# Kernel tuning notes

Measured on AMD Instinct MI355X. Metric: run time of the kernel, lower is better.

The kernel has to match this reference:

```python
import jax, jax.numpy as jnp
import numpy as np

B, E, H, N_TAYLOR = 8192, 256, 4096, 4
BN_EPS = 1e-5


def setup_inputs() -> dict:
    key = jax.random.key(0)
    ks = jax.random.split(key, 6)
    s = 0.02
    return {
        "z1": jax.random.normal(ks[0], (B, E), jnp.float32),
        "z2": jax.random.normal(ks[1], (B, E), jnp.float32),
        "p1": jax.random.normal(ks[2], (B, E), jnp.float32),
        "p2": jax.random.normal(ks[3], (B, E), jnp.float32),
        "W1": jax.random.normal(ks[4], (E, H), jnp.float32) * s,
        "gamma": jnp.ones((H,), jnp.float32),
        "beta": jnp.zeros((H,), jnp.float32),
        "W2": jax.random.normal(ks[5], (H, E), jnp.float32) * s,
        "b2": jnp.zeros((E,), jnp.float32),
        "lamda_inv": jnp.asarray(100.0, jnp.float32),
    }


def _predictor(z, W1, gamma, beta, W2, b2):
    h = z @ W1                                   # [B, H]
    mu = jnp.mean(h, axis=0)
    var = jnp.mean(jnp.square(h - mu), axis=0)   # biased var (torch BN training)
    h = (h - mu) * jax.lax.rsqrt(var + BN_EPS) * gamma + beta
    h = jax.nn.relu(h)
    return h @ W2 + b2                           # [B, E]


def _l2norm(x):
    n = jnp.linalg.norm(x, axis=1, keepdims=True)
    return x / jnp.maximum(n, 1e-12)


def _mec(view1, view2, lamda_inv):
    v1, v2 = _l2norm(view1), _l2norm(view2)
    c = (v1 @ v2.T) / lamda_inv                  # [B, B]
    power = c
    sum_p = jnp.zeros_like(c)
    for k in range(1, N_TAYLOR + 1):
        if k > 1:
            power = power @ c
        sign = 1.0 if (k + 1) % 2 == 0 else -1.0
        sum_p = sum_p + sign * power / k
    return jnp.trace(sum_p)


def reference(z1, z2, p1, p2, W1, gamma, beta, W2, b2, lamda_inv):
    q1 = _predictor(z1, W1, gamma, beta, W2, b2)
    q2 = _predictor(z2, W1, gamma, beta, W2, b2)
    loss = (_mec(p1, q2, lamda_inv) + _mec(p2, q1, lamda_inv)) * 0.5 / B
    return -loss * lamda_inv
```

## Files before the change

kernel.cpp:

```cpp
#include <hip/hip_runtime.h>

#define B_ROWS 8192
#define E_DIM  256
#define H_DIM  4096

typedef __attribute__((ext_vector_type(8))) short short8;
typedef __attribute__((ext_vector_type(4))) float f32x4;

typedef __attribute__((address_space(1))) const void* gas1_t;
typedef __attribute__((address_space(3))) void*       las3_t;

__device__ __forceinline__ float b2f(unsigned short s) {
    return __uint_as_float(((unsigned)s) << 16);
}
__device__ __forceinline__ unsigned short f2b(float f) {
    unsigned u = __float_as_uint(f);
    u += 0x7fffu + ((u >> 16) & 1u);
    return (unsigned short)(u >> 16);
}

__device__ __forceinline__ int swz(int row, int slot) {
    return slot ^ ((row >> 1) & 3);
}

__global__ void k_transpose_cast(const float* __restrict__ in,
                                 unsigned short* __restrict__ out,
                                 int R, int C) {
    __shared__ float tile[32][33];
    const int c0 = blockIdx.x * 32, r0 = blockIdx.y * 32;
    const int tx = threadIdx.x & 31, ty = threadIdx.x >> 5;
#pragma unroll
    for (int j = 0; j < 4; ++j)
        tile[ty * 4 + j][tx] = in[(size_t)(r0 + ty * 4 + j) * C + c0 + tx];
    __syncthreads();
#pragma unroll
    for (int j = 0; j < 4; ++j)
        out[(size_t)(c0 + ty * 4 + j) * R + r0 + tx] = f2b(tile[tx][ty * 4 + j]);
}

__global__ void k_cast_bf16(const float* __restrict__ in,
                            unsigned short* __restrict__ out, int n4) {
    int i = blockIdx.x * blockDim.x + threadIdx.x;
    if (i < n4) {
        float4 v = ((const float4*)in)[i];
        ushort4 o;
        o.x = f2b(v.x); o.y = f2b(v.y); o.z = f2b(v.z); o.w = f2b(v.w);
        ((ushort4*)out)[i] = o;
    }
}

__global__ __launch_bounds__(256) void k_gemm1(
    const unsigned short* __restrict__ A, const unsigned short* __restrict__ Bt,
    unsigned short* __restrict__ Cout,
    float* __restrict__ cs, float* __restrict__ cs2,
    int M, int N, int K) {
    constexpr int BK = 32, BM = 128, BN = 128;
    constexpr int MI = 4, NI = 4;
    __shared__ __align__(16) short As[BM * BK];
    __shared__ __align__(16) short Bs[BN * BK];

    const int t = threadIdx.x;
    const int lane = t & 63, wv = t >> 6;
    const int wr = wv >> 1, wc = wv & 1;
    const int l15 = lane & 15, quad = lane >> 4;
    const int m0 = blockIdx.y * BM, n0 = blockIdx.x * BN;

    f32x4 acc[MI][NI] = {};

    for (int k0 = 0; k0 < K; k0 += BK) {
#pragma unroll
        for (int q = 0; q < 2; ++q) {
            int u = q * 256 + t;
            int row = u >> 2, kc = swz(row, u & 3);
            const short* gp = (const short*)A + (size_t)(m0 + row) * K + k0 + kc * 8;
            short* lp = As + (size_t)(q * 256 + (wv << 6)) * 8;
            __builtin_amdgcn_global_load_lds((gas1_t)gp, (las3_t)lp, 16, 0, 0);
        }
#pragma unroll
        for (int q = 0; q < 2; ++q) {
            int u = q * 256 + t;
            int row = u >> 2, kc = swz(row, u & 3);
            const short* gp = (const short*)Bt + (size_t)(n0 + row) * K + k0 + kc * 8;
            short* lp = Bs + (size_t)(q * 256 + (wv << 6)) * 8;
            __builtin_amdgcn_global_load_lds((gas1_t)gp, (las3_t)lp, 16, 0, 0);
        }
        __syncthreads();

        short8 af[MI], bfr[NI];
#pragma unroll
        for (int mi = 0; mi < MI; ++mi) {
            int row = wr * 64 + mi * 16 + l15;
            af[mi] = *(const short8*)(As + row * BK + (swz(row, quad) << 3));
        }
#pragma unroll
        for (int ni = 0; ni < NI; ++ni) {
            int row = wc * 64 + ni * 16 + l15;
            bfr[ni] = *(const short8*)(Bs + row * BK + (swz(row, quad) << 3));
        }
#pragma unroll
        for (int mi = 0; mi < MI; ++mi)
#pragma unroll
            for (int ni = 0; ni < NI; ++ni)
                acc[mi][ni] = __builtin_amdgcn_mfma_f32_16x16x32_bf16(
                    af[mi], bfr[ni], acc[mi][ni], 0, 0, 0);
        __syncthreads();
    }

#pragma unroll
    for (int ni = 0; ni < NI; ++ni) {
        float s = 0.f, s2 = 0.f;
#pragma unroll
        for (int mi = 0; mi < MI; ++mi)
#pragma unroll
            for (int r = 0; r < 4; ++r) {
                int row = m0 + wr * 64 + mi * 16 + quad * 4 + r;
                int col = n0 + wc * 64 + ni * 16 + l15;
                float v = acc[mi][ni][r];
                Cout[(size_t)row * N + col] = f2b(v);
                s += v; s2 += v * v;
            }
        s  += __shfl_xor(s, 16);  s  += __shfl_xor(s, 32);
        s2 += __shfl_xor(s2, 16); s2 += __shfl_xor(s2, 32);
        if (quad == 0) {
            int col = n0 + wc * 64 + ni * 16 + l15;
            atomicAdd(&cs[col], s);
            atomicAdd(&cs2[col], s2);
        }
    }
}

__global__ void k_bnprep(const float* __restrict__ sum, const float* __restrict__ sumsq,
                         const float* __restrict__ gamma, const float* __restrict__ beta,
                         unsigned* __restrict__ ssb) {
    int j = blockIdx.x * 256 + threadIdx.x;
    float mu = sum[j] * (1.f / B_ROWS);
    float var = sumsq[j] * (1.f / B_ROWS) - mu * mu;
    float sc = gamma[j] * rsqrtf(var + 1e-5f);
    float sh = beta[j] - mu * sc;
    ssb[j] = ((unsigned)f2b(sc) << 16) | (unsigned)f2b(sh);
}

__device__ __forceinline__ short8 bnrelu8(uint4 hv, uint4 sa, uint4 sb) {
    const unsigned short* hu = (const unsigned short*)&hv;
    const unsigned* wa = (const unsigned*)&sa;
    const unsigned* wb = (const unsigned*)&sb;
    short8 o;
#pragma unroll
    for (int j = 0; j < 8; ++j) {
        unsigned w = j < 4 ? wa[j] : wb[j - 4];
        float sc = __uint_as_float(w & 0xffff0000u);
        float sh = __uint_as_float(w << 16);
        float v = fmaxf(b2f(hu[j]) * sc + sh, 0.f);
        o[j] = (short)f2b(v);
    }
    return o;
}

__global__ __launch_bounds__(256) void k_gemm2d(
    const unsigned short* __restrict__ A, const unsigned short* __restrict__ Bt,
    float* __restrict__ Cout, const float* __restrict__ bias,
    const unsigned* __restrict__ ssb,
    int M, int N, int K) {
    constexpr int BK = 32, BM = 64, BN = 128;
    constexpr int MI = 2, NI = 4;
    __shared__ __align__(16) short As[2][BM * BK];
    __shared__ __align__(16) short Bs[2][BN * BK];

    const int t = threadIdx.x;
    const int lane = t & 63, wv = t >> 6;
    const int wr = wv >> 1, wc = wv & 1;
    const int l15 = lane & 15, quad = lane >> 4;
    const int m0 = blockIdx.y * BM, n0 = blockIdx.x * BN;

    const int Kc = K / gridDim.z;
    const int kbeg = blockIdx.z * Kc;
    const int ITERS = Kc / BK;

    const int arow = t >> 2, akc = t & 3;
    const unsigned short* hp = A + (size_t)(m0 + arow) * K + akc * 8;
    const unsigned* ssp = ssb + akc * 8;
    const int awoff = arow * BK + (swz(arow, akc) << 3);

    const unsigned short* bp0 = Bt + (size_t)(n0 + arow) * K + akc * 8;
    const unsigned short* bp1 = Bt + (size_t)(n0 + 64 + arow) * K + akc * 8;
    const int bwoff0 = arow * BK + (swz(arow, akc) << 3);
    const int bwoff1 = (64 + arow) * BK + (swz(64 + arow, akc) << 3);

    f32x4 acc[MI][NI] = {};

    uint4 hreg = *(const uint4*)(hp + kbeg);
    uint4 sa = *(const uint4*)(ssp + kbeg);
    uint4 sb = *(const uint4*)(ssp + kbeg + 4);
    uint4 b0 = *(const uint4*)(bp0 + kbeg);
    uint4 b1 = *(const uint4*)(bp1 + kbeg);

    for (int i = 0; i < ITERS; ++i) {
        const int k0 = kbeg + i * BK;
        short* Ab = As[i & 1];
        short* Bb = Bs[i & 1];

        *(short8*)(Ab + awoff) = bnrelu8(hreg, sa, sb);
        *(uint4*)(Bb + bwoff0) = b0;
        *(uint4*)(Bb + bwoff1) = b1;
        __syncthreads();

        const int kn = (i + 1 < ITERS) ? k0 + BK : kbeg;
        hreg = *(const uint4*)(hp + kn);
        sa = *(const uint4*)(ssp + kn);
        sb = *(const uint4*)(ssp + kn + 4);
        b0 = *(const uint4*)(bp0 + kn);
        b1 = *(const uint4*)(bp1 + kn);

        short8 af[MI], bfr[NI];
#pragma unroll
        for (int mi = 0; mi < MI; ++mi) {
            int row = wr * 32 + mi * 16 + l15;
            af[mi] = *(const short8*)(Ab + row * BK + (swz(row, quad) << 3));
        }
#pragma unroll
        for (int ni = 0; ni < NI; ++ni) {
            int row = wc * 64 + ni * 16 + l15;
            bfr[ni] = *(const short8*)(Bb + row * BK + (swz(row, quad) << 3));
        }
#pragma unroll
        for (int mi = 0; mi < MI; ++mi)
#pragma unroll
            for (int ni = 0; ni < NI; ++ni)
                acc[mi][ni] = __builtin_amdgcn_mfma_f32_16x16x32_bf16(
                    af[mi], bfr[ni], acc[mi][ni], 0, 0, 0);
    }

#pragma unroll
    for (int mi = 0; mi < MI; ++mi)
#pragma unroll
        for (int ni = 0; ni < NI; ++ni)
#pragma unroll
            for (int r = 0; r < 4; ++r) {
                int row = m0 + wr * 32 + mi * 16 + quad * 4 + r;
                int col = n0 + wc * 64 + ni * 16 + l15;
                float v = acc[mi][ni][r];
                if (blockIdx.z == 0) v += bias[col];
                atomicAdd(&Cout[(size_t)row * N + col], v);
            }
}

__global__ void k_rownorm4(const float* __restrict__ a0, const float* __restrict__ a1,
                           const float* __restrict__ a2, const float* __restrict__ a3,
                           float* __restrict__ o0, float* __restrict__ o1,
                           float* __restrict__ o2, float* __restrict__ o3) {
    int which = blockIdx.y;
    const float* x = which == 0 ? a0 : which == 1 ? a1 : which == 2 ? a2 : a3;
    float* inv = which == 0 ? o0 : which == 1 ? o1 : which == 2 ? o2 : o3;
    int row = blockIdx.x * 4 + (threadIdx.x >> 6);
    int lane = threadIdx.x & 63;
    float4 v = ((const float4*)(x + (size_t)row * E_DIM))[lane];
    float s = v.x * v.x + v.y * v.y + v.z * v.z + v.w * v.w;
#pragma unroll
    for (int o = 32; o; o >>= 1) s += __shfl_down(s, o);
    if (lane == 0) inv[row] = 1.f / fmaxf(sqrtf(s), 1e-12f);
}

__global__ void k_tn_cast(
    const float* __restrict__ x0, const float* __restrict__ x1,
    const float* __restrict__ x2, const float* __restrict__ x3,
    const float* __restrict__ i0, const float* __restrict__ i1,
    const float* __restrict__ i2, const float* __restrict__ i3,
    unsigned short* __restrict__ o0, unsigned short* __restrict__ o1,
    unsigned short* __restrict__ o2, unsigned short* __restrict__ o3) {
    const int z = blockIdx.z;
    const float* x = z == 0 ? x0 : z == 1 ? x1 : z == 2 ? x2 : x3;
    const float* inv = z == 0 ? i0 : z == 1 ? i1 : z == 2 ? i2 : i3;
    unsigned short* out = z == 0 ? o0 : z == 1 ? o1 : z == 2 ? o2 : o3;

    __shared__ float tile[32][33];
    const int c0 = blockIdx.x * 32, r0 = blockIdx.y * 32;
    const int tx = threadIdx.x & 31, ty = threadIdx.x >> 5;
#pragma unroll
    for (int j = 0; j < 4; ++j) {
        int r = r0 + ty * 4 + j;
        tile[ty * 4 + j][tx] = x[(size_t)r * E_DIM + c0 + tx] * inv[r];
    }
    __syncthreads();
#pragma unroll
    for (int j = 0; j < 4; ++j)
        out[(size_t)(c0 + ty * 4 + j) * B_ROWS + r0 + tx] = f2b(tile[tx][ty * 4 + j]);
}

#define GKS 16
__global__ __launch_bounds__(256) void k_gram(
    const unsigned short* __restrict__ p1T, const unsigned short* __restrict__ q2T,
    const unsigned short* __restrict__ p2T, const unsigned short* __restrict__ q1T,
    float* __restrict__ Ma, float* __restrict__ Mb) {
    constexpr int BK = 32;
    const int mec = blockIdx.z >> 4, kz = blockIdx.z & 15;
    const unsigned short* A = mec ? p2T : p1T;
    const unsigned short* Bt = mec ? q1T : q2T;
    float* Mout = mec ? Mb : Ma;

    __shared__ __align__(16) short As[64 * BK];
    __shared__ __align__(16) short Bs[64 * BK];

    const int t = threadIdx.x;
    const int lane = t & 63, wv = t >> 6;
    const int wr = wv >> 1, wc = wv & 1;
    const int l15 = lane & 15, quad = lane >> 4;
    const int m0 = blockIdx.y * 64, n0 = blockIdx.x * 64;
    const int kbeg = kz * (B_ROWS / GKS);

    f32x4 acc[2][2] = {};

    for (int k0 = kbeg; k0 < kbeg + B_ROWS / GKS; k0 += BK) {
        {
            int row = t >> 2, kc = swz(row, t & 3);
            const short* gpa = (const short*)A + (size_t)(m0 + row) * B_ROWS + k0 + kc * 8;
            short* lpa = As + (size_t)(wv << 6) * 8;
            __builtin_amdgcn_global_load_lds((gas1_t)gpa, (las3_t)lpa, 16, 0, 0);
            const short* gpb = (const short*)Bt + (size_t)(n0 + row) * B_ROWS + k0 + kc * 8;
            short* lpb = Bs + (size_t)(wv << 6) * 8;
            __builtin_amdgcn_global_load_lds((gas1_t)gpb, (las3_t)lpb, 16, 0, 0);
        }
        __syncthreads();

        short8 af[2], bfr[2];
#pragma unroll
        for (int mi = 0; mi < 2; ++mi) {
            int row = wr * 32 + mi * 16 + l15;
            af[mi] = *(const short8*)(As + row * BK + (swz(row, quad) << 3));
        }
#pragma unroll
        for (int ni = 0; ni < 2; ++ni) {
            int row = wc * 32 + ni * 16 + l15;
            bfr[ni] = *(const short8*)(Bs + row * BK + (swz(row, quad) << 3));
        }
#pragma unroll
        for (int mi = 0; mi < 2; ++mi)
#pragma unroll
            for (int ni = 0; ni < 2; ++ni)
                acc[mi][ni] = __builtin_amdgcn_mfma_f32_16x16x32_bf16(
                    af[mi], bfr[ni], acc[mi][ni], 0, 0, 0);
        __syncthreads();
    }

#pragma unroll
    for (int mi = 0; mi < 2; ++mi)
#pragma unroll
        for (int ni = 0; ni < 2; ++ni)
#pragma unroll
            for (int r = 0; r < 4; ++r) {
                int row = m0 + wr * 32 + mi * 16 + quad * 4 + r;
                int col = n0 + wc * 32 + ni * 16 + l15;
                atomicAdd(&Mout[(size_t)row * E_DIM + col], acc[mi][ni][r]);
            }
}

__global__ void k_m2(const float* __restrict__ Ma, const float* __restrict__ Mb,
                     float* __restrict__ M2a, float* __restrict__ M2b) {
    const float* M = blockIdx.z ? Mb : Ma;
    float* M2 = blockIdx.z ? M2b : M2a;
    int b = blockIdx.x * 16 + (threadIdx.x & 15);
    int a = blockIdx.y * 16 + (threadIdx.x >> 4);
    float s = 0.f;
    for (int k = 0; k < E_DIM; ++k) s += M[a * E_DIM + k] * M[k * E_DIM + b];
    M2[a * E_DIM + b] = s;
}

__global__ __launch_bounds__(256) void k_traces2(
    const float* __restrict__ Ma, const float* __restrict__ M2a,
    const float* __restrict__ Mb, const float* __restrict__ M2b,
    const float* __restrict__ lam, float* __restrict__ out) {
    const float* M  = blockIdx.z ? Mb  : Ma;
    const float* M2 = blockIdx.z ? M2b : M2a;
    const int i0 = blockIdx.y * 32, j0 = blockIdx.x * 32;
    const int t = threadIdx.x, col = t & 31, row = t >> 5;

    __shared__ float A[32][33], Bt[32][33], A2[32][33], B2[32][33];
#pragma unroll
    for (int r = 0; r < 4; ++r) {
        int rr = r * 8 + row;
        A [rr][col] = M [(i0 + rr) * E_DIM + j0 + col];
        Bt[rr][col] = M [(j0 + rr) * E_DIM + i0 + col];
        A2[rr][col] = M2[(i0 + rr) * E_DIM + j0 + col];
        B2[rr][col] = M2[(j0 + rr) * E_DIM + i0 + col];
    }
    __syncthreads();

    float lamv = lam[0];
    float il = 1.f / lamv;
    float F = -0.5f * lamv * (1.f / B_ROWS);
    float c1 = F * il;
    float c2 = -F * 0.5f * il * il;
    float c3 = F * (1.f / 3.f) * il * il * il;
    float c4 = -F * 0.25f * il * il * il * il;

    float s = 0.f;
#pragma unroll
    for (int r = 0; r < 4; ++r) {
        int rr = r * 8 + row;
        float mij = A[rr][col], mji = Bt[col][rr];
        float m2ij = A2[rr][col], m2ji = B2[col][rr];
        s += c2 * mij * mji + c3 * m2ij * mji + c4 * m2ij * m2ji;
        if (i0 + rr == j0 + col) s += c1 * mij;
    }
#pragma unroll
    for (int o = 32; o; o >>= 1) s += __shfl_down(s, o);
    __shared__ float red[4];
    if ((t & 63) == 0) red[t >> 6] = s;
    __syncthreads();
    if (t == 0) atomicAdd(out, red[0] + red[1] + red[2] + red[3]);
}

extern "C" void kernel_launch(void* const* d_in, const int* in_sizes, int n_in,
                              void* d_out, int out_size, void* d_ws, size_t ws_size,
                              hipStream_t stream) {
    const float* z1 = (const float*)d_in[0];
    const float* z2 = (const float*)d_in[1];
    const float* p1 = (const float*)d_in[2];
    const float* p2 = (const float*)d_in[3];
    const float* W1 = (const float*)d_in[4];
    const float* gamma = (const float*)d_in[5];
    const float* beta = (const float*)d_in[6];
    const float* W2 = (const float*)d_in[7];
    const float* b2 = (const float*)d_in[8];
    const float* lam = (const float*)d_in[9];
    float* out = (float*)d_out;
    char* ws = (char*)d_ws;

    size_t off = 0;
    auto alloc = [&](size_t bytes) { size_t o = off; off += (bytes + 255) & ~(size_t)255; return o; };
    unsigned short* W1T = (unsigned short*)(ws + alloc((size_t)E_DIM * H_DIM * 2));
    unsigned short* W2T = (unsigned short*)(ws + alloc((size_t)H_DIM * E_DIM * 2));
    unsigned short* zb  = (unsigned short*)(ws + alloc((size_t)B_ROWS * E_DIM * 2));
    unsigned short* h   = (unsigned short*)(ws + alloc((size_t)B_ROWS * H_DIM * 2));
    float* q1 = (float*)(ws + alloc((size_t)B_ROWS * E_DIM * 4));
    float* q2 = (float*)(ws + alloc((size_t)B_ROWS * E_DIM * 4));
    float* colsum   = (float*)(ws + alloc(H_DIM * 4));
    float* colsumsq = (float*)(ws + alloc(H_DIM * 4));
    unsigned* ssb = (unsigned*)(ws + alloc(H_DIM * 4));
    float* invp1 = (float*)(ws + alloc(B_ROWS * 4));
    float* invp2 = (float*)(ws + alloc(B_ROWS * 4));
    float* invq1 = (float*)(ws + alloc(B_ROWS * 4));
    float* invq2 = (float*)(ws + alloc(B_ROWS * 4));
    float* Ma  = (float*)(ws + alloc((size_t)E_DIM * E_DIM * 4));
    float* Mb  = (float*)(ws + alloc((size_t)E_DIM * E_DIM * 4));
    float* M2a = (float*)(ws + alloc((size_t)E_DIM * E_DIM * 4));
    float* M2b = (float*)(ws + alloc((size_t)E_DIM * E_DIM * 4));

    const size_t TSZ = (size_t)E_DIM * B_ROWS;
    unsigned short* p1T = h;
    unsigned short* q2T = h + TSZ;
    unsigned short* p2T = h + 2 * TSZ;
    unsigned short* q1T = h + 3 * TSZ;

    hipMemsetAsync(out, 0, sizeof(float), stream);
    hipMemsetAsync(q1, 0, (size_t)2 * B_ROWS * E_DIM * sizeof(float), stream);

    k_transpose_cast<<<dim3(H_DIM / 32, E_DIM / 32), 256, 0, stream>>>(W1, W1T, E_DIM, H_DIM);
    k_transpose_cast<<<dim3(E_DIM / 32, H_DIM / 32), 256, 0, stream>>>(W2, W2T, H_DIM, E_DIM);

    const float* zs[2] = {z1, z2};
    float* qs[2] = {q1, q2};
    for (int v = 0; v < 2; ++v) {
        k_cast_bf16<<<dim3(B_ROWS * E_DIM / 4 / 256), 256, 0, stream>>>(zs[v], zb, B_ROWS * E_DIM / 4);
        hipMemsetAsync(colsum, 0, H_DIM * 2 * sizeof(float), stream);
        k_gemm1<<<dim3(H_DIM / 128, B_ROWS / 128), 256, 0, stream>>>(
            zb, W1T, h, colsum, colsumsq, B_ROWS, H_DIM, E_DIM);
        k_bnprep<<<dim3(H_DIM / 256), 256, 0, stream>>>(colsum, colsumsq, gamma, beta, ssb);
        k_gemm2d<<<dim3(E_DIM / 128, B_ROWS / 64, 4), 256, 0, stream>>>(
            h, W2T, qs[v], b2, ssb, B_ROWS, E_DIM, H_DIM);
    }

    k_rownorm4<<<dim3(B_ROWS / 4, 4), 256, 0, stream>>>(p1, p2, q1, q2, invp1, invp2, invq1, invq2);

    k_tn_cast<<<dim3(E_DIM / 32, B_ROWS / 32, 4), 256, 0, stream>>>(
        p1, q2, p2, q1, invp1, invq2, invp2, invq1, p1T, q2T, p2T, q1T);

    hipMemsetAsync(Ma, 0, (size_t)E_DIM * E_DIM * 2 * sizeof(float), stream);
    k_gram<<<dim3(4, 4, 2 * GKS), 256, 0, stream>>>(p1T, q2T, p2T, q1T, Ma, Mb);
    k_m2<<<dim3(16, 16, 2), 256, 0, stream>>>(Ma, Mb, M2a, M2b);
    k_traces2<<<dim3(8, 8, 2), 256, 0, stream>>>(Ma, M2a, Mb, M2b, lam, out);
}
```

Baseline: 345.0 us.

## Fuse z bf16 cast into GEMM1 and widen GEMM2 tile to full E

Drops the separate fp32-to-bf16 cast kernel for z and converts inside GEMM1 while staging through double-buffered LDS with register prefetch, replacing the async global_load_lds path. GEMM2 now uses a 64x256 tile covering the whole output width, so each H tile and its BN/ReLU transform is loaded once instead of twice. Split-K goes from 4 to 8 to keep the grid occupied. The cost is more fp32 atomics on the output and higher register and LDS use per block.

```diff
diff --git a/kernel.cpp b/kernel.cpp
--- a/kernel.cpp
+++ b/kernel.cpp
@@ -21,6 +21,15 @@
 
 __device__ __forceinline__ int swz(int row, int slot) {
     return slot ^ ((row >> 1) & 3);
+}
+
+__device__ __forceinline__ short8 pack8(float4 a, float4 b) {
+    short8 o;
+    o[0] = (short)f2b(a.x); o[1] = (short)f2b(a.y);
+    o[2] = (short)f2b(a.z); o[3] = (short)f2b(a.w);
+    o[4] = (short)f2b(b.x); o[5] = (short)f2b(b.y);
+    o[6] = (short)f2b(b.z); o[7] = (short)f2b(b.w);
+    return o;
 }
 
 __global__ void k_transpose_cast(const float* __restrict__ in,
@@ -38,26 +47,13 @@
         out[(size_t)(c0 + ty * 4 + j) * R + r0 + tx] = f2b(tile[tx][ty * 4 + j]);
 }
 
-__global__ void k_cast_bf16(const float* __restrict__ in,
-                            unsigned short* __restrict__ out, int n4) {
-    int i = blockIdx.x * blockDim.x + threadIdx.x;
-    if (i < n4) {
-        float4 v = ((const float4*)in)[i];
-        ushort4 o;
-        o.x = f2b(v.x); o.y = f2b(v.y); o.z = f2b(v.z); o.w = f2b(v.w);
-        ((ushort4*)out)[i] = o;
-    }
-}
-
-__global__ __launch_bounds__(256) void k_gemm1(
-    const unsigned short* __restrict__ A, const unsigned short* __restrict__ Bt,
-    unsigned short* __restrict__ Cout,
-    float* __restrict__ cs, float* __restrict__ cs2,
-    int M, int N, int K) {
-    constexpr int BK = 32, BM = 128, BN = 128;
-    constexpr int MI = 4, NI = 4;
-    __shared__ __align__(16) short As[BM * BK];
-    __shared__ __align__(16) short Bs[BN * BK];
+__global__ __launch_bounds__(256) void k_gemm1d(
+    const float* __restrict__ Z, const unsigned short* __restrict__ Bt,
+    unsigned short* __restrict__ Hout,
+    float* __restrict__ cs, float* __restrict__ cs2) {
+    constexpr int BK = 32, BM = 128, BN = 128, K = E_DIM, ITERS = K / BK;
+    __shared__ __align__(16) short As[2][BM * BK];
+    __shared__ __align__(16) short Bs[2][BN * BK];
 
     const int t = threadIdx.x;
     const int lane = t & 63, wv = t >> 6;
@@ -65,58 +61,64 @@
     const int l15 = lane & 15, quad = lane >> 4;
     const int m0 = blockIdx.y * BM, n0 = blockIdx.x * BN;
 
-    f32x4 acc[MI][NI] = {};
-
-    for (int k0 = 0; k0 < K; k0 += BK) {
-#pragma unroll
-        for (int q = 0; q < 2; ++q) {
-            int u = q * 256 + t;
-            int row = u >> 2, kc = swz(row, u & 3);
-            const short* gp = (const short*)A + (size_t)(m0 + row) * K + k0 + kc * 8;
-            short* lp = As + (size_t)(q * 256 + (wv << 6)) * 8;
-            __builtin_amdgcn_global_load_lds((gas1_t)gp, (las3_t)lp, 16, 0, 0);
-        }
-#pragma unroll
-        for (int q = 0; q < 2; ++q) {
-            int u = q * 256 + t;
-            int row = u >> 2, kc = swz(row, u & 3);
-            const short* gp = (const short*)Bt + (size_t)(n0 + row) * K + k0 + kc * 8;
-            short* lp = Bs + (size_t)(q * 256 + (wv << 6)) * 8;
-            __builtin_amdgcn_global_load_lds((gas1_t)gp, (las3_t)lp, 16, 0, 0);
-        }
+    const int r0 = t >> 2, akc = t & 3;
+    const float* zp0 = Z + (size_t)(m0 + r0) * K + akc * 8;
+    const float* zp1 = Z + (size_t)(m0 + 64 + r0) * K + akc * 8;
+    const unsigned short* bp0 = Bt + (size_t)(n0 + r0) * K + akc * 8;
+    const unsigned short* bp1 = Bt + (size_t)(n0 + 64 + r0) * K + akc * 8;
+    const int aw0 = r0 * BK + (swz(r0, akc) << 3);
+    const int aw1 = (64 + r0) * BK + (swz(64 + r0, akc) << 3);
+
+    f32x4 acc[4][4] = {};
+
+    float4 a00 = *(const float4*)(zp0),     a01 = *(const float4*)(zp0 + 4);
+    float4 a10 = *(const float4*)(zp1),     a11 = *(const float4*)(zp1 + 4);
+    uint4  b0  = *(const uint4*)(bp0),      b1  = *(const uint4*)(bp1);
+
+    for (int i = 0; i < ITERS; ++i) {
+        short* Ab = As[i & 1];
+        short* Bb = Bs[i & 1];
+        *(short8*)(Ab + aw0) = pack8(a00, a01);
+        *(short8*)(Ab + aw1) = pack8(a10, a11);
+        *(uint4*)(Bb + aw0) = b0;
+        *(uint4*)(Bb + aw1) = b1;
         __syncthreads();
 
-        short8 af[MI], bfr[NI];
-#pragma unroll
-        for (int mi = 0; mi < MI; ++mi) {
+        const int kn = (i + 1 < ITERS) ? (i + 1) * BK : 0;
+        a00 = *(const float4*)(zp0 + kn); a01 = *(const float4*)(zp0 + kn + 4);
+        a10 = *(const float4*)(zp1 + kn); a11 = *(const float4*)(zp1 + kn + 4);
+        b0 = *(const uint4*)(bp0 + kn);   b1 = *(const uint4*)(bp1 + kn);
+
+        short8 af[4], bfr[4];
+#pragma unroll
+        for (int mi = 0; mi < 4; ++mi) {
             int row = wr * 64 + mi * 16 + l15;
-            af[mi] = *(const short8*)(As + row * BK + (swz(row, quad) << 3));
-        }
-#pragma unroll
-        for (int ni = 0; ni < NI; ++ni) {
+            af[mi] = *(const short8*)(Ab + row * BK + (swz(row, quad) << 3));
+        }
+#pragma unroll
+        for (int ni = 0; ni < 4; ++ni) {
             int row = wc * 64 + ni * 16 + l15;
-            bfr[ni] = *(const short8*)(Bs + row * BK + (swz(row, quad) << 3));
-        }
-#pragma unroll
-        for (int mi = 0; mi < MI; ++mi)
-#pragma unroll
-            for (int ni = 0; ni < NI; ++ni)
+            bfr[ni] = *(const short8*)(Bb + row * BK + (swz(row, quad) << 3));
+        }
+#pragma unroll
+        for (int mi = 0; mi < 4; ++mi)
+#pragma unroll
+            for (int ni = 0; ni < 4; ++ni)
                 acc[mi][ni] = __builtin_amdgcn_mfma_f32_16x16x32_bf16(
                     af[mi], bfr[ni], acc[mi][ni], 0, 0, 0);
-        __syncthreads();
-    }
-
-#pragma unroll
-    for (int ni = 0; ni < NI; ++ni) {
+    }
+
+#pragma unroll
+    for (int ni = 0; ni < 4; ++ni) {
         float s = 0.f, s2 = 0.f;
 #pragma unroll
-        for (int mi = 0; mi < MI; ++mi)
+        for (int mi = 0; mi < 4; ++mi)
 #pragma unroll
             for (int r = 0; r < 4; ++r) {
                 int row = m0 + wr * 64 + mi * 16 + quad * 4 + r;
                 int col = n0 + wc * 64 + ni * 16 + l15;
                 float v = acc[mi][ni][r];
-                Cout[(size_t)row * N + col] = f2b(v);
+                Hout[(size_t)row * H_DIM + col] = f2b(v);
                 s += v; s2 += v * v;
             }
         s  += __shfl_xor(s, 16);  s  += __shfl_xor(s, 32);
@@ -156,91 +158,94 @@
     return o;
 }
 
-__global__ __launch_bounds__(256) void k_gemm2d(
-    const unsigned short* __restrict__ A, const unsigned short* __restrict__ Bt,
+__global__ __launch_bounds__(256) void k_gemm2w(
+    const unsigned short* __restrict__ H, const unsigned short* __restrict__ Bt,
     float* __restrict__ Cout, const float* __restrict__ bias,
-    const unsigned* __restrict__ ssb,
-    int M, int N, int K) {
-    constexpr int BK = 32, BM = 64, BN = 128;
-    constexpr int MI = 2, NI = 4;
+    const unsigned* __restrict__ ssb) {
+    constexpr int BK = 32, BM = 64, BN = 256, K = H_DIM;
     __shared__ __align__(16) short As[2][BM * BK];
     __shared__ __align__(16) short Bs[2][BN * BK];
 
     const int t = threadIdx.x;
     const int lane = t & 63, wv = t >> 6;
-    const int wr = wv >> 1, wc = wv & 1;
     const int l15 = lane & 15, quad = lane >> 4;
-    const int m0 = blockIdx.y * BM, n0 = blockIdx.x * BN;
+    const int m0 = blockIdx.y * BM;
+    const int nw = wv * 64;
 
     const int Kc = K / gridDim.z;
     const int kbeg = blockIdx.z * Kc;
     const int ITERS = Kc / BK;
 
-    const int arow = t >> 2, akc = t & 3;
-    const unsigned short* hp = A + (size_t)(m0 + arow) * K + akc * 8;
+    const int r0 = t >> 2, akc = t & 3;
+    const unsigned short* hp = H + (size_t)(m0 + r0) * K + akc * 8;
     const unsigned* ssp = ssb + akc * 8;
-    const int awoff = arow * BK + (swz(arow, akc) << 3);
-
-    const unsigned short* bp0 = Bt + (size_t)(n0 + arow) * K + akc * 8;
-    const unsigned short* bp1 = Bt + (size_t)(n0 + 64 + arow) * K + akc * 8;
-    const int bwoff0 = arow * BK + (swz(arow, akc) << 3);
-    const int bwoff1 = (64 + arow) * BK + (swz(64 + arow, akc) << 3);
-
-    f32x4 acc[MI][NI] = {};
+    const int aw = r0 * BK + (swz(r0, akc) << 3);
+
+    const unsigned short* bp[4];
+    int bw[4];
+#pragma unroll
+    for (int j = 0; j < 4; ++j) {
+        int row = j * 64 + r0;
+        bp[j] = Bt + (size_t)row * K + akc * 8;
+        bw[j] = row * BK + (swz(row, akc) << 3);
+    }
+
+    f32x4 acc[4][4] = {};
 
     uint4 hreg = *(const uint4*)(hp + kbeg);
     uint4 sa = *(const uint4*)(ssp + kbeg);
     uint4 sb = *(const uint4*)(ssp + kbeg + 4);
-    uint4 b0 = *(const uint4*)(bp0 + kbeg);
-    uint4 b1 = *(const uint4*)(bp1 + kbeg);
+    uint4 breg[4];
+#pragma unroll
+    for (int j = 0; j < 4; ++j) breg[j] = *(const uint4*)(bp[j] + kbeg);
 
     for (int i = 0; i < ITERS; ++i) {
         const int k0 = kbeg + i * BK;
         short* Ab = As[i & 1];
         short* Bb = Bs[i & 1];
 
-        *(short8*)(Ab + awoff) = bnrelu8(hreg, sa, sb);
-        *(uint4*)(Bb + bwoff0) = b0;
-        *(uint4*)(Bb + bwoff1) = b1;
+        *(short8*)(Ab + aw) = bnrelu8(hreg, sa, sb);
+#pragma unroll
+        for (int j = 0; j < 4; ++j) *(uint4*)(Bb + bw[j]) = breg[j];
         __syncthreads();
 
         const int kn = (i + 1 < ITERS) ? k0 + BK : kbeg;
         hreg = *(const uint4*)(hp + kn);
         sa = *(const uint4*)(ssp + kn);
         sb = *(const uint4*)(ssp + kn + 4);
-        b0 = *(const uint4*)(bp0 + kn);
-        b1 = *(const uint4*)(bp1 + kn);
-
-        short8 af[MI], bfr[NI];
-#pragma unroll
-        for (int mi = 0; mi < MI; ++mi) {
-            int row = wr * 32 + mi * 16 + l15;
+#pragma unroll
+        for (int j = 0; j < 4; ++j) breg[j] = *(const uint4*)(bp[j] + kn);
+
+        short8 af[4], bfr[4];
+#pragma unroll
+        for (int mi = 0; mi < 4; ++mi) {
+            int row = mi * 16 + l15;
             af[mi] = *(const short8*)(Ab + row * BK + (swz(row, quad) << 3));
         }
 #pragma unroll
-        for (int ni = 0; ni < NI; ++ni) {
-            int row = wc * 64 + ni * 16 + l15;
+        for (int ni = 0; ni < 4; ++ni) {
+            int row = nw + ni * 16 + l15;
             bfr[ni] = *(const short8*)(Bb + row * BK + (swz(row, quad) << 3));
         }
 #pragma unroll
-        for (int mi = 0; mi < MI; ++mi)
-#pragma unroll
-            for (int ni = 0; ni < NI; ++ni)
+        for (int mi = 0; mi < 4; ++mi)
+#pragma unroll
+            for (int ni = 0; ni < 4; ++ni)
                 acc[mi][ni] = __builtin_amdgcn_mfma_f32_16x16x32_bf16(
                     af[mi], bfr[ni], acc[mi][ni], 0, 0, 0);
     }
 
 #pragma unroll
-    for (int mi = 0; mi < MI; ++mi)
-#pragma unroll
-        for (int ni = 0; ni < NI; ++ni)
+    for (int mi = 0; mi < 4; ++mi)
+#pragma unroll
+        for (int ni = 0; ni < 4; ++ni)
 #pragma unroll
             for (int r = 0; r < 4; ++r) {
-                int row = m0 + wr * 32 + mi * 16 + quad * 4 + r;
-                int col = n0 + wc * 64 + ni * 16 + l15;
+                int row = m0 + mi * 16 + quad * 4 + r;
+                int col = nw + ni * 16 + l15;
                 float v = acc[mi][ni][r];
                 if (blockIdx.z == 0) v += bias[col];
-                atomicAdd(&Cout[(size_t)row * N + col], v);
+                atomicAdd(&Cout[(size_t)row * E_DIM + col], v);
             }
 }
 
@@ -429,7 +434,6 @@
     auto alloc = [&](size_t bytes) { size_t o = off; off += (bytes + 255) & ~(size_t)255; return o; };
     unsigned short* W1T = (unsigned short*)(ws + alloc((size_t)E_DIM * H_DIM * 2));
     unsigned short* W2T = (unsigned short*)(ws + alloc((size_t)H_DIM * E_DIM * 2));
-    unsigned short* zb  = (unsigned short*)(ws + alloc((size_t)B_ROWS * E_DIM * 2));
     unsigned short* h   = (unsigned short*)(ws + alloc((size_t)B_ROWS * H_DIM * 2));
     float* q1 = (float*)(ws + alloc((size_t)B_ROWS * E_DIM * 4));
     float* q2 = (float*)(ws + alloc((size_t)B_ROWS * E_DIM * 4));
@@ -460,13 +464,12 @@
     const float* zs[2] = {z1, z2};
     float* qs[2] = {q1, q2};
     for (int v = 0; v < 2; ++v) {
-        k_cast_bf16<<<dim3(B_ROWS * E_DIM / 4 / 256), 256, 0, stream>>>(zs[v], zb, B_ROWS * E_DIM / 4);
         hipMemsetAsync(colsum, 0, H_DIM * 2 * sizeof(float), stream);
-        k_gemm1<<<dim3(H_DIM / 128, B_ROWS / 128), 256, 0, stream>>>(
-            zb, W1T, h, colsum, colsumsq, B_ROWS, H_DIM, E_DIM);
+        k_gemm1d<<<dim3(H_DIM / 128, B_ROWS / 128), 256, 0, stream>>>(
+            zs[v], W1T, h, colsum, colsumsq);
         k_bnprep<<<dim3(H_DIM / 256), 256, 0, stream>>>(colsum, colsumsq, gamma, beta, ssb);
-        k_gemm2d<<<dim3(E_DIM / 128, B_ROWS / 64, 4), 256, 0, stream>>>(
-            h, W2T, qs[v], b2, ssb, B_ROWS, E_DIM, H_DIM);
+        k_gemm2w<<<dim3(1, B_ROWS / 64, 8), 256, 0, stream>>>(
+            h, W2T, qs[v], b2, ssb);
     }
 
     k_rownorm4<<<dim3(B_ROWS / 4, 4), 256, 0, stream>>>(p1, p2, q1, q2, invp1, invp2, invq1, invq2);
```

After: 525.5 us. 52.3% more time.

## Fuse input cast into GEMM1, fuse rownorm with transpose-cast, merge memsets

Applied to the files above, without the earlier changes.

GEMM1 now reads fp32 z directly, converts it to bf16 while staging into LDS, and covers all of K=256 in two 128-wide chunks, which removes the separate cast kernel and the bf16 z buffer. The row-norm and transpose-cast kernels are merged into one kernel that loads 32 full rows, computes their inverse norms in shared memory, and writes the normalized transposed bf16 output. The memsets are consolidated by relying on Ma/Mb sitting right after q1/q2 in the workspace, and colsum buffers are split per view. The costs are larger LDS tiles (64KB per block, lowering occupancy), non-async A loads in GEMM1, and a layout-dependent memset.

```diff
diff --git a/kernel.cpp b/kernel.cpp
--- a/kernel.cpp
+++ b/kernel.cpp
@@ -21,6 +21,15 @@
 
 __device__ __forceinline__ int swz(int row, int slot) {
     return slot ^ ((row >> 1) & 3);
+}
+
+__device__ __forceinline__ short8 pack8(float4 a, float4 b) {
+    short8 o;
+    o[0] = (short)f2b(a.x); o[1] = (short)f2b(a.y);
+    o[2] = (short)f2b(a.z); o[3] = (short)f2b(a.w);
+    o[4] = (short)f2b(b.x); o[5] = (short)f2b(b.y);
+    o[6] = (short)f2b(b.z); o[7] = (short)f2b(b.w);
+    return o;
 }
 
 __global__ void k_transpose_cast(const float* __restrict__ in,
@@ -38,85 +47,85 @@
         out[(size_t)(c0 + ty * 4 + j) * R + r0 + tx] = f2b(tile[tx][ty * 4 + j]);
 }
 
-__global__ void k_cast_bf16(const float* __restrict__ in,
-                            unsigned short* __restrict__ out, int n4) {
-    int i = blockIdx.x * blockDim.x + threadIdx.x;
-    if (i < n4) {
-        float4 v = ((const float4*)in)[i];
-        ushort4 o;
-        o.x = f2b(v.x); o.y = f2b(v.y); o.z = f2b(v.z); o.w = f2b(v.w);
-        ((ushort4*)out)[i] = o;
-    }
-}
-
-__global__ __launch_bounds__(256) void k_gemm1(
-    const unsigned short* __restrict__ A, const unsigned short* __restrict__ Bt,
-    unsigned short* __restrict__ Cout,
-    float* __restrict__ cs, float* __restrict__ cs2,
-    int M, int N, int K) {
-    constexpr int BK = 32, BM = 128, BN = 128;
-    constexpr int MI = 4, NI = 4;
-    __shared__ __align__(16) short As[BM * BK];
-    __shared__ __align__(16) short Bs[BN * BK];
+__global__ __launch_bounds__(256) void k_gemm1b(
+    const float* __restrict__ Z, const unsigned short* __restrict__ Bt,
+    unsigned short* __restrict__ Hout,
+    float* __restrict__ cs, float* __restrict__ cs2) {
+    constexpr int K = E_DIM;
+    constexpr int KC = 128;
+    __shared__ __align__(16) short As[128 * KC];
+    __shared__ __align__(16) short Bs[128 * KC];
 
     const int t = threadIdx.x;
     const int lane = t & 63, wv = t >> 6;
     const int wr = wv >> 1, wc = wv & 1;
     const int l15 = lane & 15, quad = lane >> 4;
-    const int m0 = blockIdx.y * BM, n0 = blockIdx.x * BN;
-
-    f32x4 acc[MI][NI] = {};
-
-    for (int k0 = 0; k0 < K; k0 += BK) {
-#pragma unroll
-        for (int q = 0; q < 2; ++q) {
-            int u = q * 256 + t;
-            int row = u >> 2, kc = swz(row, u & 3);
-            const short* gp = (const short*)A + (size_t)(m0 + row) * K + k0 + kc * 8;
-            short* lp = As + (size_t)(q * 256 + (wv << 6)) * 8;
+    const int m0 = blockIdx.y * 128, n0 = blockIdx.x * 128;
+
+    f32x4 acc[4][4] = {};
+
+#pragma unroll
+    for (int half = 0; half < 2; ++half) {
+        const int kh = half * KC;
+        if (half) __syncthreads();
+
+#pragma unroll
+        for (int i = 0; i < 8; ++i) {
+            int u = i * 256 + t;
+            int row = u >> 4, pos = u & 15;
+            int c = pos ^ (row & 7);
+            const short* gp = (const short*)Bt + (size_t)(n0 + row) * K + kh + c * 8;
+            short* lp = Bs + (size_t)(i * 256 + (wv << 6)) * 8;
             __builtin_amdgcn_global_load_lds((gas1_t)gp, (las3_t)lp, 16, 0, 0);
         }
-#pragma unroll
-        for (int q = 0; q < 2; ++q) {
-            int u = q * 256 + t;
-            int row = u >> 2, kc = swz(row, u & 3);
-            const short* gp = (const short*)Bt + (size_t)(n0 + row) * K + k0 + kc * 8;
-            short* lp = Bs + (size_t)(q * 256 + (wv << 6)) * 8;
-            __builtin_amdgcn_global_load_lds((gas1_t)gp, (las3_t)lp, 16, 0, 0);
+        {
+            int row = t >> 1;
+            int cbase = (t & 1) * 8;
+#pragma unroll
+            for (int j = 0; j < 8; ++j) {
+                int c = cbase + j;
+                const float* zp = Z + (size_t)(m0 + row) * K + kh + c * 8;
+                float4 a = *(const float4*)zp;
+                float4 b = *(const float4*)(zp + 4);
+                *(short8*)(As + row * KC + ((c ^ (row & 7)) << 3)) = pack8(a, b);
+            }
         }
         __syncthreads();
 
-        short8 af[MI], bfr[NI];
-#pragma unroll
-        for (int mi = 0; mi < MI; ++mi) {
-            int row = wr * 64 + mi * 16 + l15;
-            af[mi] = *(const short8*)(As + row * BK + (swz(row, quad) << 3));
-        }
-#pragma unroll
-        for (int ni = 0; ni < NI; ++ni) {
-            int row = wc * 64 + ni * 16 + l15;
-            bfr[ni] = *(const short8*)(Bs + row * BK + (swz(row, quad) << 3));
-        }
-#pragma unroll
-        for (int mi = 0; mi < MI; ++mi)
-#pragma unroll
-            for (int ni = 0; ni < NI; ++ni)
-                acc[mi][ni] = __builtin_amdgcn_mfma_f32_16x16x32_bf16(
-                    af[mi], bfr[ni], acc[mi][ni], 0, 0, 0);
-        __syncthreads();
-    }
-
-#pragma unroll
-    for (int ni = 0; ni < NI; ++ni) {
+#pragma unroll
+        for (int s = 0; s < 4; ++s) {
+            int cc = s * 4 + quad;
+            short8 af[4], bfr[4];
+#pragma unroll
+            for (int mi = 0; mi < 4; ++mi) {
+                int row = wr * 64 + mi * 16 + l15;
+                af[mi] = *(const short8*)(As + row * KC + ((cc ^ (row & 7)) << 3));
+            }
+#pragma unroll
+            for (int ni = 0; ni < 4; ++ni) {
+                int row = wc * 64 + ni * 16 + l15;
+                bfr[ni] = *(const short8*)(Bs + row * KC + ((cc ^ (row & 7)) << 3));
+            }
+#pragma unroll
+            for (int mi = 0; mi < 4; ++mi)
+#pragma unroll
+                for (int ni = 0; ni < 4; ++ni)
+                    acc[mi][ni] = __builtin_amdgcn_mfma_f32_16x16x32_bf16(
+                        af[mi], bfr[ni], acc[mi][ni], 0, 0, 0);
+        }
+    }
+
+#pragma unroll
+    for (int ni = 0; ni < 4; ++ni) {
         float s = 0.f, s2 = 0.f;
 #pragma unroll
-        for (int mi = 0; mi < MI; ++mi)
+        for (int mi = 0; mi < 4; ++mi)
 #pragma unroll
             for (int r = 0; r < 4; ++r) {
                 int row = m0 + wr * 64 + mi * 16 + quad * 4 + r;
                 int col = n0 + wc * 64 + ni * 16 + l15;
                 float v = acc[mi][ni][r];
-                Cout[(size_t)row * N + col] = f2b(v);
+                Hout[(size_t)row * H_DIM + col] = f2b(v);
                 s += v; s2 += v * v;
             }
         s  += __shfl_xor(s, 16);  s  += __shfl_xor(s, 32);
@@ -244,46 +253,53 @@
             }
 }
 
-__global__ void k_rownorm4(const float* __restrict__ a0, const float* __restrict__ a1,
-                           const float* __restrict__ a2, const float* __restrict__ a3,
-                           float* __restrict__ o0, float* __restrict__ o1,
-                           float* __restrict__ o2, float* __restrict__ o3) {
-    int which = blockIdx.y;
-    const float* x = which == 0 ? a0 : which == 1 ? a1 : which == 2 ? a2 : a3;
-    float* inv = which == 0 ? o0 : which == 1 ? o1 : which == 2 ? o2 : o3;
-    int row = blockIdx.x * 4 + (threadIdx.x >> 6);
-    int lane = threadIdx.x & 63;
-    float4 v = ((const float4*)(x + (size_t)row * E_DIM))[lane];
-    float s = v.x * v.x + v.y * v.y + v.z * v.z + v.w * v.w;
-#pragma unroll
-    for (int o = 32; o; o >>= 1) s += __shfl_down(s, o);
-    if (lane == 0) inv[row] = 1.f / fmaxf(sqrtf(s), 1e-12f);
-}
-
-__global__ void k_tn_cast(
+__global__ __launch_bounds__(256) void k_ntc(
     const float* __restrict__ x0, const float* __restrict__ x1,
     const float* __restrict__ x2, const float* __restrict__ x3,
-    const float* __restrict__ i0, const float* __restrict__ i1,
-    const float* __restrict__ i2, const float* __restrict__ i3,
     unsigned short* __restrict__ o0, unsigned short* __restrict__ o1,
     unsigned short* __restrict__ o2, unsigned short* __restrict__ o3) {
-    const int z = blockIdx.z;
+    const int z = blockIdx.y;
     const float* x = z == 0 ? x0 : z == 1 ? x1 : z == 2 ? x2 : x3;
-    const float* inv = z == 0 ? i0 : z == 1 ? i1 : z == 2 ? i2 : i3;
     unsigned short* out = z == 0 ? o0 : z == 1 ? o1 : z == 2 ? o2 : o3;
 
-    __shared__ float tile[32][33];
-    const int c0 = blockIdx.x * 32, r0 = blockIdx.y * 32;
-    const int tx = threadIdx.x & 31, ty = threadIdx.x >> 5;
-#pragma unroll
-    for (int j = 0; j < 4; ++j) {
-        int r = r0 + ty * 4 + j;
-        tile[ty * 4 + j][tx] = x[(size_t)r * E_DIM + c0 + tx] * inv[r];
-    }
-    __syncthreads();
-#pragma unroll
-    for (int j = 0; j < 4; ++j)
-        out[(size_t)(c0 + ty * 4 + j) * B_ROWS + r0 + tx] = f2b(tile[tx][ty * 4 + j]);
+    __shared__ float tile[32][264];
+    __shared__ float red[32][8];
+    __shared__ float invs[32];
+    const int t = threadIdx.x;
+    const int r0 = blockIdx.x * 32;
+
+#pragma unroll
+    for (int i = 0; i < 8; ++i) {
+        int u = i * 256 + t;
+        int row = u >> 6, cp = (u & 63) * 4;
+        float4 v = *(const float4*)(x + (size_t)(r0 + row) * E_DIM + cp);
+        *(float4*)&tile[row][cp] = v;
+    }
+    __syncthreads();
+    {
+        int row = t >> 3, cg = (t & 7) * 32;
+        float s = 0.f;
+#pragma unroll
+        for (int j = 0; j < 32; ++j) { float v = tile[row][cg + j]; s += v * v; }
+        red[row][t & 7] = s;
+    }
+    __syncthreads();
+    if (t < 32) {
+        float s = 0.f;
+#pragma unroll
+        for (int j = 0; j < 8; ++j) s += red[t][j];
+        invs[t] = 1.f / fmaxf(sqrtf(s), 1e-12f);
+    }
+    __syncthreads();
+    {
+        int row = t & 31, cb = (t >> 5) * 32;
+        float inv = invs[row];
+#pragma unroll
+        for (int j = 0; j < 32; ++j) {
+            int c = cb + j;
+            out[(size_t)c * B_ROWS + r0 + row] = f2b(tile[row][c] * inv);
+        }
+    }
 }
 
 #define GKS 16
@@ -429,21 +445,18 @@
     auto alloc = [&](size_t bytes) { size_t o = off; off += (bytes + 255) & ~(size_t)255; return o; };
     unsigned short* W1T = (unsigned short*)(ws + alloc((size_t)E_DIM * H_DIM * 2));
     unsigned short* W2T = (unsigned short*)(ws + alloc((size_t)H_DIM * E_DIM * 2));
-    unsigned short* zb  = (unsigned short*)(ws + alloc((size_t)B_ROWS * E_DIM * 2));
     unsigned short* h   = (unsigned short*)(ws + alloc((size_t)B_ROWS * H_DIM * 2));
     float* q1 = (float*)(ws + alloc((size_t)B_ROWS * E_DIM * 4));
     float* q2 = (float*)(ws + alloc((size_t)B_ROWS * E_DIM * 4));
-    float* colsum   = (float*)(ws + alloc(H_DIM * 4));
-    float* colsumsq = (float*)(ws + alloc(H_DIM * 4));
-    unsigned* ssb = (unsigned*)(ws + alloc(H_DIM * 4));
-    float* invp1 = (float*)(ws + alloc(B_ROWS * 4));
-    float* invp2 = (float*)(ws + alloc(B_ROWS * 4));
-    float* invq1 = (float*)(ws + alloc(B_ROWS * 4));
-    float* invq2 = (float*)(ws + alloc(B_ROWS * 4));
     float* Ma  = (float*)(ws + alloc((size_t)E_DIM * E_DIM * 4));
     float* Mb  = (float*)(ws + alloc((size_t)E_DIM * E_DIM * 4));
     float* M2a = (float*)(ws + alloc((size_t)E_DIM * E_DIM * 4));
     float* M2b = (float*)(ws + alloc((size_t)E_DIM * E_DIM * 4));
+    float* cs0 = (float*)(ws + alloc(H_DIM * 4));
+    float* cs0q = (float*)(ws + alloc(H_DIM * 4));
+    float* cs1 = (float*)(ws + alloc(H_DIM * 4));
+    float* cs1q = (float*)(ws + alloc(H_DIM * 4));
+    unsigned* ssb = (unsigned*)(ws + alloc(H_DIM * 4));
 
     const size_t TSZ = (size_t)E_DIM * B_ROWS;
     unsigned short* p1T = h;
@@ -452,29 +465,27 @@
     unsigned short* q1T = h + 3 * TSZ;
 
     hipMemsetAsync(out, 0, sizeof(float), stream);
-    hipMemsetAsync(q1, 0, (size_t)2 * B_ROWS * E_DIM * sizeof(float), stream);
+    hipMemsetAsync(q1, 0, ((size_t)2 * B_ROWS * E_DIM + 2 * E_DIM * E_DIM) * 4, stream);
+    hipMemsetAsync(cs0, 0, (size_t)4 * H_DIM * 4, stream);
 
     k_transpose_cast<<<dim3(H_DIM / 32, E_DIM / 32), 256, 0, stream>>>(W1, W1T, E_DIM, H_DIM);
     k_transpose_cast<<<dim3(E_DIM / 32, H_DIM / 32), 256, 0, stream>>>(W2, W2T, H_DIM, E_DIM);
 
     const float* zs[2] = {z1, z2};
     float* qs[2] = {q1, q2};
+    float* css[2] = {cs0, cs1};
+    float* cssq[2] = {cs0q, cs1q};
     for (int v = 0; v < 2; ++v) {
-        k_cast_bf16<<<dim3(B_ROWS * E_DIM / 4 / 256), 256, 0, stream>>>(zs[v], zb, B_ROWS * E_DIM / 4);
-        hipMemsetAsync(colsum, 0, H_DIM * 2 * sizeof(float), stream);
-        k_gemm1<<<dim3(H_DIM / 128, B_ROWS / 128), 256, 0, stream>>>(
-            zb, W1T, h, colsum, colsumsq, B_ROWS, H_DIM, E_DIM);
-        k_bnprep<<<dim3(H_DIM / 256), 256, 0, stream>>>(colsum, colsumsq, gamma, beta, ssb);
+        k_gemm1b<<<dim3(H_DIM / 128, B_ROWS / 128), 256, 0, stream>>>(
+            zs[v], W1T, h, css[v], cssq[v]);
+        k_bnprep<<<dim3(H_DIM / 256), 256, 0, stream>>>(css[v], cssq[v], gamma, beta, ssb);
         k_gemm2d<<<dim3(E_DIM / 128, B_ROWS / 64, 4), 256, 0, stream>>>(
             h, W2T, qs[v], b2, ssb, B_ROWS, E_DIM, H_DIM);
     }
 
-    k_rownorm4<<<dim3(B_ROWS / 4, 4), 256, 0, stream>>>(p1, p2, q1, q2, invp1, invp2, invq1, invq2);
-
-    k_tn_cast<<<dim3(E_DIM / 32, B_ROWS / 32, 4), 256, 0, stream>>>(
-        p1, q2, p2, q1, invp1, invq2, invp2, invq1, p1T, q2T, p2T, q1T);
-
-    hipMemsetAsync(Ma, 0, (size_t)E_DIM * E_DIM * 2 * sizeof(float), stream);
+    k_ntc<<<dim3(B_ROWS / 32, 4), 256, 0, stream>>>(
+        p1, q2, p2, q1, p1T, q2T, p2T, q1T);
+
     k_gram<<<dim3(4, 4, 2 * GKS), 256, 0, stream>>>(p1T, q2T, p2T, q1T, Ma, Mb);
     k_m2<<<dim3(16, 16, 2), 256, 0, stream>>>(Ma, Mb, M2a, M2b);
     k_traces2<<<dim3(8, 8, 2), 256, 0, stream>>>(Ma, M2a, Mb, M2b, lam, out);
```

New measurement: 374.8 us. +8.7%, slower.
